# Kernel tuning notes

Measured on AMD Instinct MI355X. Metric: run time of the kernel, lower is better.

## Reference

```python
import jax, jax.numpy as jnp
import numpy as np

B, S, H, NH, NE = 4, 1024, 256, 4, 4
D = H // NH  # head_unit = 64
EPS = 1e-8


def layernorm(x, g, b):
    m = jnp.mean(x, axis=-1, keepdims=True)
    v = jnp.mean((x - m) ** 2, axis=-1, keepdims=True)
    return (x - m) / jnp.sqrt(v + EPS) * g + b


def setup_inputs() -> dict:
    key = jax.random.key(0)
    ks = jax.random.split(key, 18)
    sc = 0.05
    return {
        "x": jax.random.normal(ks[0], (B, S, H), jnp.float32),
        # MoEMultiHead params
        "hl_w": jax.random.normal(ks[1], (NH, D, H), jnp.float32) * sc,   # head_layer weights (out,in)
        "hl_b": jax.random.normal(ks[2], (NH, D), jnp.float32) * sc,
        "wq": jax.random.normal(ks[3], (NH, NE, D, D), jnp.float32) * sc,  # w_q[i*NH+j] -> wq[i,j]
        "wk": jax.random.normal(ks[4], (NH, D, D), jnp.float32) * sc,
        "wv": jax.random.normal(ks[5], (NH, D, D), jnp.float32) * sc,
        "gate_w": jax.random.normal(ks[6], (NH, NE, NE * D), jnp.float32) * sc,
        "gate_b": jax.random.normal(ks[7], (NH, NE), jnp.float32) * sc,
        "ln_g": jnp.ones((D,), jnp.float32),
        "ln_b": jnp.zeros((D,), jnp.float32),
        # FFN params (built inside forward in torch; materialized here)
        "fc1_w": jax.random.normal(ks[8], (D, D), jnp.float32) * sc,
        "fc1_b": jax.random.normal(ks[9], (D,), jnp.float32) * sc,
        "fc2_w": jax.random.normal(ks[10], (D, D), jnp.float32) * sc,
        "fc2_b": jax.random.normal(ks[11], (D,), jnp.float32) * sc,
        "fnorm_g": jnp.ones((D,), jnp.float32),
        "fnorm_b": jnp.zeros((D,), jnp.float32),
        "fgate_w": jax.random.normal(ks[12], (NH, H), jnp.float32) * sc,
    }


def reference(x, hl_w, hl_b, wq, wk, wv, gate_w, gate_b, ln_g, ln_b,
              fc1_w, fc1_b, fc2_w, fc2_b, fnorm_g, fnorm_b, fgate_w):
    b, s, h = x.shape
    nh, d, _ = wk.shape
    ne = wq.shape[1]
    # per-head projection of full hidden -> head_unit  (B, NH, S, D)
    sx = jnp.einsum('bsh,ndh->bnsd', x, hl_w) + hl_b[None, :, None, :]
    pad = sx == 0  # padding mask, same for all experts
    # per-(head, expert) q; per-head k, v
    q = jnp.einsum('bnsd,neod->bneso', sx, wq)       # (B,NH,NE,S,D)
    k = jnp.einsum('bnsd,nod->bnso', sx, wk)         # (B,NH,S,D)
    v = jnp.einsum('bnsd,nod->bnso', sx, wv)
    causal = jnp.where(jnp.tril(jnp.ones((s, s), bool)), 0.0, -jnp.inf).astype(x.dtype)
    # NOTE: original MULTIPLIES by sqrt(head_unit) (bug-faithful)
    scores = jnp.einsum('bnesd,bntd->bnest', q, k) * (d ** 0.5) + causal
    att = jax.nn.softmax(scores, axis=-1)
    qkv = jnp.einsum('bnest,bntd->bnesd', att, v)
    qkv = jnp.where(pad[:, :, None], 0.0, qkv)
    # concat experts along feature dim: (B,NH,S,NE*D)
    out = jnp.transpose(qkv, (0, 1, 3, 2, 4)).reshape(b, nh, s, ne * d)
    gs = jax.nn.softmax(jnp.einsum('bnsf,nef->bnse', out, gate_w) + gate_b[None, :, None, :], axis=-1)
    mixed = jnp.einsum('bnsed,bnse->bnsd', out.reshape(b, nh, s, ne, d), gs)
    # bug-faithful residual: split_x[i] indexes the BATCH dim with head index i
    resid = sx[jnp.arange(nh), jnp.arange(nh)]  # (NH, S, D), broadcast over batch
    hn = layernorm(mixed + resid, ln_g, ln_b)   # (B,NH,S,D); dropout inactive (p=0)
    f_n = jnp.transpose(hn, (0, 2, 1, 3)).reshape(b, s, h)
    # ---- FFN (fresh module in torch; deterministic params here) ----
    fx = f_n.reshape(b, s, nh, d)  # torch.split along feature dim
    pm = fx == 0
    hx = jnp.where(pm, 0.0, fx @ fc1_w.T + fc1_b)
    hx = jax.nn.relu(hx)
    hx = jnp.where(pm, 0.0, hx @ fc2_w.T + fc2_b)
    hx = layernorm(hx + fx, fnorm_g, fnorm_b)
    fout = hx.reshape(b, s, h)
    fg = jax.nn.softmax(fout @ fgate_w.T, axis=-1)  # (B,S,NH)
    return (fout.reshape(b, s, nh, d) * fg[..., None]).reshape(b, s, h)
```

## Files before the change

### kernel.cpp

```cpp
#include <hip/hip_runtime.h>
#include <math.h>

typedef unsigned short u16;
typedef __attribute__((ext_vector_type(8))) unsigned short us8;
typedef __attribute__((ext_vector_type(4))) unsigned short us4;
typedef __attribute__((ext_vector_type(8))) short bf16x8;
typedef __attribute__((ext_vector_type(4))) float f32x4;

constexpr int B_ = 4, S_ = 1024, H_ = 256, NH_ = 4, NE_ = 4, D_ = 64;
constexpr float EPS_ = 1e-8f;

__device__ __forceinline__ u16 f2bf(float f){
  unsigned u = __float_as_uint(f);
  unsigned rnd = 0x7fffu + ((u>>16)&1u);
  return (u16)((u + rnd)>>16);
}
__device__ __forceinline__ us8 pack8(float4 a, float4 b){
  us8 r;
  r[0]=f2bf(a.x); r[1]=f2bf(a.y); r[2]=f2bf(a.z); r[3]=f2bf(a.w);
  r[4]=f2bf(b.x); r[5]=f2bf(b.y); r[6]=f2bf(b.z); r[7]=f2bf(b.w);
  return r;
}
#define MFMA16(a,b,c) __builtin_amdgcn_mfma_f32_16x16x32_bf16((bf16x8)(a),(bf16x8)(b),(c),0,0,0)

__global__ __launch_bounds__(256) void k_sx(const float* __restrict__ x, const float* __restrict__ hlw,
                                            const float* __restrict__ hlb,
                                            float* __restrict__ sx, u16* __restrict__ sxb){
  int mt = blockIdx.x >> 3, nt = blockIdx.x & 7;
  int tid = threadIdx.x, w = tid>>6, l = tid&63, lr = l>>4, lc = l&15;
  __shared__ u16 Xs[64*64];
  __shared__ u16 Ws[32*64];
  const int swl = (lc&7)<<3;
  f32x4 acc[2] = {{0,0,0,0},{0,0,0,0}};
  for(int ks=0; ks<4; ++ks){
    __syncthreads();
    #pragma unroll
    for(int it=0; it<2; ++it){
      int c0 = w*8 + it*32;
      const float* xp = x + ((size_t)(mt*64+l))*H_ + ks*64 + c0;
      float4 a = *(const float4*)xp, b = *(const float4*)(xp+4);
      *(us8*)&Xs[l*64 + (c0 ^ ((l&7)<<3))] = pack8(a,b);
    }
    { int row = tid&31, c0 = (tid>>5)*8;
      const float* wp = hlw + ((size_t)(nt*32+row))*H_ + ks*64 + c0;
      float4 a = *(const float4*)wp, b = *(const float4*)(wp+4);
      *(us8*)&Ws[row*64 + (c0 ^ ((row&7)<<3))] = pack8(a,b);
    }
    __syncthreads();
    bf16x8 a0 = *(const bf16x8*)&Xs[(w*16+lc)*64 + ((lr*8   ) ^ swl)];
    bf16x8 a1 = *(const bf16x8*)&Xs[(w*16+lc)*64 + ((lr*8+32) ^ swl)];
    #pragma unroll
    for(int j=0;j<2;j++){
      const u16* wr = &Ws[(j*16+lc)*64];
      bf16x8 b0 = *(const bf16x8*)(wr + ((lr*8   ) ^ swl));
      bf16x8 b1 = *(const bf16x8*)(wr + ((lr*8+32) ^ swl));
      acc[j] = MFMA16(a0,b0,acc[j]);
      acc[j] = MFMA16(a1,b1,acc[j]);
    }
  }
  #pragma unroll
  for(int j=0;j<2;j++){
    int col = nt*32 + j*16 + lc;
    int n = col>>6, d = col&63;
    float bias = hlb[col];
    #pragma unroll
    for(int r=0;r<4;r++){
      int m = mt*64 + w*16 + lr*4 + r;
      int b = m>>10, s = m&1023;
      float v = acc[j][r] + bias;
      size_t idx = ((size_t)(b*NH_+n)*S_ + s)*D_ + d;
      sx[idx] = v; sxb[idx] = f2bf(v);
    }
  }
}

__global__ __launch_bounds__(256) void k_qkv(const u16* __restrict__ sxb, const float* __restrict__ wq,
            const float* __restrict__ wk, const float* __restrict__ wv,
            u16* __restrict__ qb, u16* __restrict__ kbf, u16* __restrict__ vbf){
  int bid = blockIdx.x;
  int half = bid&1, mt = (bid>>1)&63, n = bid>>7;
  int tid = threadIdx.x, w = tid>>6, l = tid&63, lr = l>>4, lc = l&15;
  __shared__ u16 As[64*64];
  __shared__ u16 Ws[192*64];
  const int swl = (lc&7)<<3;
  int b = (mt*64)>>10, s0 = (mt*64)&1023;
  #pragma unroll
  for(int it=0; it<2; ++it){
    int c0 = w*8 + it*32;
    us8 v = *(const us8*)(sxb + ((size_t)(b*NH_+n)*S_ + s0 + l)*D_ + c0);
    *(us8*)&As[l*64 + (c0 ^ ((l&7)<<3))] = v;
  }
  #pragma unroll
  for(int ch=0; ch<3; ++ch){
    int o = half*192 + ch*64 + l;
    const float* src;
    if(o < 256)      src = wq + ((size_t)((n*NE_ + (o>>6))*D_ + (o&63)))*D_;
    else if(o < 320) src = wk + ((size_t)(n*D_ + (o-256)))*D_;
    else             src = wv + ((size_t)(n*D_ + (o-320)))*D_;
    #pragma unroll
    for(int it=0; it<2; ++it){
      int c0 = w*8 + it*32;
      float4 a = *(const float4*)(src+c0), bb = *(const float4*)(src+c0+4);
      *(us8*)&Ws[(ch*64+l)*64 + (c0 ^ ((l&7)<<3))] = pack8(a,bb);
    }
  }
  __syncthreads();
  bf16x8 a0 = *(const bf16x8*)&As[(w*16+lc)*64 + ((lr*8   ) ^ swl)];
  bf16x8 a1 = *(const bf16x8*)&As[(w*16+lc)*64 + ((lr*8+32) ^ swl)];
  f32x4 acc[12];
  #pragma unroll
  for(int j=0;j<12;j++) acc[j] = (f32x4){0,0,0,0};
  #pragma unroll
  for(int j=0;j<12;j++){
    const u16* wr = &Ws[(j*16+lc)*64];
    bf16x8 b0 = *(const bf16x8*)(wr + ((lr*8   ) ^ swl));
    bf16x8 b1 = *(const bf16x8*)(wr + ((lr*8+32) ^ swl));
    acc[j] = MFMA16(a0,b0,acc[j]);
    acc[j] = MFMA16(a1,b1,acc[j]);
  }
  #pragma unroll
  for(int j=0;j<12;j++){
    int o = half*192 + j*16 + lc;
    #pragma unroll
    for(int r=0;r<4;r++){
      int s = s0 + w*16 + lr*4 + r;
      float v = acc[j][r];
      if(o < 256){
        int e = o>>6, d = o&63;
        qb[((size_t)((b*NH_+n)*NE_+e)*S_ + s)*D_ + d] = f2bf(v*8.f);
      } else if(o < 320){
        kbf[((size_t)(b*NH_+n)*S_ + s)*D_ + (o-256)] = f2bf(v);
      } else {
        vbf[((size_t)(b*NH_+n)*S_ + s)*D_ + (o-320)] = f2bf(v);
      }
    }
  }
}

__global__ __launch_bounds__(256) void k_attn(const u16* __restrict__ qb, const u16* __restrict__ kb,
        const u16* __restrict__ vb, const float* __restrict__ sx, float* __restrict__ attout){
  int bid = blockIdx.x;
  int head = bid>>3, p = bid&7;
  int bq = head>>2, e = head&3;
  int tid = threadIdx.x, w = tid>>6, l = tid&63, lr = l>>4, lc = l&15;
  __shared__ u16 Ks[2][64*64];
  __shared__ u16 VT[2][64*64];
  __shared__ u16 Pb[4][16*64];
  const u16* kh = kb + (size_t)bq*S_*D_;
  const u16* vh = vb + (size_t)bq*S_*D_;
  const int swl = (lc&7)<<3;
  const int swst = (l&7)<<3;

  #pragma unroll
  for(int ph=0; ph<2; ++ph){
    int qt = ph ? (15-p) : p;
    const u16* qrow = qb + ((size_t)head*S_ + qt*64 + w*16 + lc)*D_;
    bf16x8 qf0 = *(const bf16x8*)(qrow + lr*8);
    bf16x8 qf1 = *(const bf16x8*)(qrow + lr*8 + 32);
    f32x4 Oa[4]; float m_i[4], l_i[4];
    #pragma unroll
    for(int j=0;j<4;j++) Oa[j] = (f32x4){0,0,0,0};
    #pragma unroll
    for(int r=0;r<4;r++){ m_i[r] = -INFINITY; l_i[r] = 0.f; }

    us8 rg[4];
    __syncthreads();
    { const u16* kr = kh + (size_t)l*D_;
      const u16* vr = vh + (size_t)l*D_;
      int c0 = w*8;
      rg[0] = *(const us8*)(kr + c0);      rg[1] = *(const us8*)(kr + c0 + 32);
      rg[2] = *(const us8*)(vr + c0);      rg[3] = *(const us8*)(vr + c0 + 32);
      *(us8*)&Ks[0][l*64 + ( c0      ^ swst)] = rg[0];
      *(us8*)&Ks[0][l*64 + ((c0+32)  ^ swst)] = rg[1];
      #pragma unroll
      for(int i=0;i<8;i++){ int d=c0+i;    VT[0][d*64 + (l ^ ((d&7)<<3))] = rg[2][i]; }
      #pragma unroll
      for(int i=0;i<8;i++){ int d=c0+32+i; VT[0][d*64 + (l ^ ((d&7)<<3))] = rg[3][i]; }
    }
    for(int kt=0; kt<=qt; ++kt){
      int cur = kt&1;
      __syncthreads();
      bool more = kt < qt;
      if(more){
        const u16* kr = kh + ((size_t)(kt+1)*64 + l)*D_;
        const u16* vr = vh + ((size_t)(kt+1)*64 + l)*D_;
        int c0 = w*8;
        rg[0] = *(const us8*)(kr + c0);    rg[1] = *(const us8*)(kr + c0 + 32);
        rg[2] = *(const us8*)(vr + c0);    rg[3] = *(const us8*)(vr + c0 + 32);
      }
      f32x4 Sa[4];
      #pragma unroll
      for(int j=0;j<4;j++){
        const u16* kr = &Ks[cur][(j*16+lc)*64];
        bf16x8 b0 = *(const bf16x8*)(kr + ((lr*8   ) ^ swl));
        bf16x8 b1 = *(const bf16x8*)(kr + ((lr*8+32) ^ swl));
        f32x4 z = (f32x4){0,0,0,0};
        z = MFMA16(qf0,b0,z);
        z = MFMA16(qf1,b1,z);
        Sa[j] = z;
      }
      #pragma unroll
      for(int r=0;r<4;r++){
        int qr = w*16 + lr*4 + r;
        float sv[4];
        #pragma unroll
        for(int j=0;j<4;j++){
          sv[j] = Sa[j][r];
          if(kt==qt && (j*16+lc) > qr) sv[j] = -INFINITY;
        }
        float mx = fmaxf(fmaxf(sv[0],sv[1]),fmaxf(sv[2],sv[3]));
        #pragma unroll
        for(int off=1; off<16; off<<=1) mx = fmaxf(mx, __shfl_xor(mx,off));
        float mn = fmaxf(m_i[r], mx);
        float sc = __expf(m_i[r]-mn);
        float rs = 0.f;
        #pragma unroll
        for(int j=0;j<4;j++){ sv[j] = __expf(sv[j]-mn); rs += sv[j]; }
        #pragma unroll
        for(int off=1; off<16; off<<=1) rs += __shfl_xor(rs,off);
        l_i[r] = l_i[r]*sc + rs;
        m_i[r] = mn;
        #pragma unroll
        for(int j=0;j<4;j++) Oa[j][r] *= sc;
        int prow = lr*4+r, psw = (prow&7)<<3;
        #pragma unroll
        for(int j=0;j<4;j++) Pb[w][prow*64 + ((j*16+lc) ^ psw)] = f2bf(sv[j]);
      }
      asm volatile("s_waitcnt lgkmcnt(0)" ::: "memory");
      bf16x8 pA0 = *(const bf16x8*)&Pb[w][lc*64 + ((lr*8   ) ^ swl)];
      bf16x8 pA1 = *(const bf16x8*)&Pb[w][lc*64 + ((lr*8+32) ^ swl)];
      #pragma unroll
      for(int jd=0;jd<4;jd++){
        const u16* vr = &VT[cur][(jd*16+lc)*64];
        bf16x8 v0 = *(const bf16x8*)(vr + ((lr*8   ) ^ swl));
        bf16x8 v1 = *(const bf16x8*)(vr + ((lr*8+32) ^ swl));
        Oa[jd] = MFMA16(pA0,v0,Oa[jd]);
        Oa[jd] = MFMA16(pA1,v1,Oa[jd]);
      }
      if(more){
        int nb = cur^1, c0 = w*8;
        *(us8*)&Ks[nb][l*64 + ( c0     ^ swst)] = rg[0];
        *(us8*)&Ks[nb][l*64 + ((c0+32) ^ swst)] = rg[1];
        #pragma unroll
        for(int i=0;i<8;i++){ int d=c0+i;    VT[nb][d*64 + (l ^ ((d&7)<<3))] = rg[2][i]; }
        #pragma unroll
        for(int i=0;i<8;i++){ int d=c0+32+i; VT[nb][d*64 + (l ^ ((d&7)<<3))] = rg[3][i]; }
      }
    }
    #pragma unroll
    for(int r=0;r<4;r++){
      int qg = qt*64 + w*16 + lr*4 + r;
      float inv = 1.f/l_i[r];
      #pragma unroll
      for(int jd=0;jd<4;jd++){
        int d = jd*16 + lc;
        float o = Oa[jd][r]*inv;
        if(sx[((size_t)bq*S_ + qg)*D_ + d] == 0.f) o = 0.f;
        attout[((size_t)bq*S_ + qg)*(NE_*D_) + e*D_ + d] = o;
      }
    }
  }
}

__global__ __launch_bounds__(256) void k_tail(const float* __restrict__ attout, const float* __restrict__ gw,
      const float* __restrict__ gb, const float* __restrict__ sx,
      const float* __restrict__ lng, const float* __restrict__ lnb,
      const float* __restrict__ w1g, const float* __restrict__ b1g,
      const float* __restrict__ w2g, const float* __restrict__ b2g,
      const float* __restrict__ fng, const float* __restrict__ fnb,
      const float* __restrict__ fgw, float* __restrict__ out){
  int bid = blockIdx.x;
  int gs0 = bid*16, b = gs0>>10, s0 = gs0&1023;
  int tid = threadIdx.x;
  int row = tid>>4, l16 = tid&15;
  int w = tid>>6, l = tid&63, lr = l>>4, lc = l&15;
  __shared__ float Fx[64][64];
  __shared__ u16 FnB[64*64];
  __shared__ u16 W1[64*64], W2[64*64], H1[64*64];
  __shared__ float Red[4][16][4];

  #pragma unroll
  for(int g2=0; g2<2; ++g2){
    int g = tid*2+g2; int r2 = g>>3, c0 = (g&7)*8;
    float4 a = *(const float4*)(w1g + r2*64 + c0), bb = *(const float4*)(w1g + r2*64 + c0 + 4);
    *(us8*)&W1[r2*64 + (c0 ^ ((r2&7)<<3))] = pack8(a,bb);
    a = *(const float4*)(w2g + r2*64 + c0); bb = *(const float4*)(w2g + r2*64 + c0 + 4);
    *(us8*)&W2[r2*64 + (c0 ^ ((r2&7)<<3))] = pack8(a,bb);
  }
  const int d0 = l16*4;
  for(int n=0;n<NH_;++n){
    f32x4 o[4];
    const float* ar = attout + ((size_t)(b*NH_+n)*S_ + s0 + row)*(NE_*D_);
    #pragma unroll
    for(int e=0;e<4;e++) o[e] = *(const f32x4*)(ar + e*64 + d0);
    float lg4[4];
    #pragma unroll
    for(int eg=0; eg<4; ++eg){
      const float* gr = gw + (size_t)(n*NE_+eg)*(NE_*D_);
      float p = 0.f;
      #pragma unroll
      for(int e=0;e<4;e++){
        f32x4 g4 = *(const f32x4*)(gr + e*64 + d0);
        p += o[e][0]*g4[0] + o[e][1]*g4[1] + o[e][2]*g4[2] + o[e][3]*g4[3];
      }
      #pragma unroll
      for(int off=1; off<16; off<<=1) p += __shfl_xor(p, off);
      lg4[eg] = p + gb[n*NE_+eg];
    }
    float mx = fmaxf(fmaxf(lg4[0],lg4[1]),fmaxf(lg4[2],lg4[3]));
    float se = 0.f;
    #pragma unroll
    for(int eg=0;eg<4;eg++){ lg4[eg]=__expf(lg4[eg]-mx); se+=lg4[eg]; }
    float inv = 1.f/se;
    f32x4 res = *(const f32x4*)(sx + ((size_t)(n*NH_+n)*S_ + s0 + row)*D_ + d0);
    float tv[4];
    #pragma unroll
    for(int k=0;k<4;k++){
      float mixk = o[0][k]*lg4[0] + o[1][k]*lg4[1] + o[2][k]*lg4[2] + o[3][k]*lg4[3];
      tv[k] = mixk*inv + res[k];
    }
    float sum = tv[0]+tv[1]+tv[2]+tv[3];
    #pragma unroll
    for(int off=1; off<16; off<<=1) sum += __shfl_xor(sum, off);
    float mean = sum*(1.f/64.f);
    float vs = 0.f;
    #pragma unroll
    for(int k=0;k<4;k++){ float d = tv[k]-mean; vs += d*d; }
    #pragma unroll
    for(int off=1; off<16; off<<=1) vs += __shfl_xor(vs, off);
    float rstd = rsqrtf(vs*(1.f/64.f)+EPS_);
    f32x4 lgv = *(const f32x4*)(lng + d0);
    f32x4 lbv = *(const f32x4*)(lnb + d0);
    int hr = n*16+row;
    us4 pk;
    f32x4 yv;
    #pragma unroll
    for(int k=0;k<4;k++){
      float y = (tv[k]-mean)*rstd*lgv[k] + lbv[k];
      yv[k] = y; pk[k] = f2bf(y);
    }
    *(f32x4*)&Fx[hr][d0] = yv;
    *(us4*)&FnB[hr*64 + (d0 ^ ((hr&7)<<3))] = pk;
  }
  __syncthreads();
  const int swl = (lc&7)<<3;
  bf16x8 a0 = *(const bf16x8*)&FnB[(w*16+lc)*64 + ((lr*8   ) ^ swl)];
  bf16x8 a1 = *(const bf16x8*)&FnB[(w*16+lc)*64 + ((lr*8+32) ^ swl)];
  f32x4 acc1[4];
  #pragma unroll
  for(int jn=0;jn<4;jn++) acc1[jn] = (f32x4){0,0,0,0};
  #pragma unroll
  for(int jn=0;jn<4;jn++){
    const u16* wr = &W1[(jn*16+lc)*64];
    bf16x8 b0 = *(const bf16x8*)(wr + ((lr*8   ) ^ swl));
    bf16x8 b1 = *(const bf16x8*)(wr + ((lr*8+32) ^ swl));
    acc1[jn] = MFMA16(a0,b0,acc1[jn]);
    acc1[jn] = MFMA16(a1,b1,acc1[jn]);
  }
  #pragma unroll
  for(int jn=0;jn<4;jn++){
    int dout = jn*16+lc;
    float bias = b1g[dout];
    #pragma unroll
    for(int rr=0;rr<4;rr++){
      int hr = w*16 + lr*4 + rr;
      float v = acc1[jn][rr] + bias;
      v = (Fx[hr][dout]==0.f) ? 0.f : v;
      v = fmaxf(v, 0.f);
      H1[hr*64 + (dout ^ ((hr&7)<<3))] = f2bf(v);
    }
  }
  __syncthreads();
  a0 = *(const bf16x8*)&H1[(w*16+lc)*64 + ((lr*8   ) ^ swl)];
  a1 = *(const bf16x8*)&H1[(w*16+lc)*64 + ((lr*8+32) ^ swl)];
  f32x4 acc2[4];
  #pragma unroll
  for(int jn=0;jn<4;jn++) acc2[jn] = (f32x4){0,0,0,0};
  #pragma unroll
  for(int jn=0;jn<4;jn++){
    const u16* wr = &W2[(jn*16+lc)*64];
    bf16x8 b0 = *(const bf16x8*)(wr + ((lr*8   ) ^ swl));
    bf16x8 b1 = *(const bf16x8*)(wr + ((lr*8+32) ^ swl));
    acc2[jn] = MFMA16(a0,b0,acc2[jn]);
    acc2[jn] = MFMA16(a1,b1,acc2[jn]);
  }
  float tv2[4][4];
  #pragma unroll
  for(int jn=0;jn<4;jn++){
    int dout = jn*16+lc;
    float bias = b2g[dout];
    #pragma unroll
    for(int rr=0;rr<4;rr++){
      int hr = w*16 + lr*4 + rr;
      float fx = Fx[hr][dout];
      float v = acc2[jn][rr] + bias;
      v = (fx==0.f) ? 0.f : v;
      tv2[jn][rr] = v + fx;
    }
  }
  float sum_r[4], vs_r[4];
  #pragma unroll
  for(int rr=0;rr<4;rr++) sum_r[rr] = tv2[0][rr]+tv2[1][rr]+tv2[2][rr]+tv2[3][rr];
  #pragma unroll
  for(int off=1; off<16; off<<=1)
    #pragma unroll
    for(int rr=0;rr<4;rr++) sum_r[rr] += __shfl_xor(sum_r[rr], off);
  float mean_r[4];
  #pragma unroll
  for(int rr=0;rr<4;rr++) mean_r[rr] = sum_r[rr]*(1.f/64.f);
  #pragma unroll
  for(int rr=0;rr<4;rr++){
    float a = tv2[0][rr]-mean_r[rr], b2v = tv2[1][rr]-mean_r[rr];
    float c = tv2[2][rr]-mean_r[rr], d = tv2[3][rr]-mean_r[rr];
    vs_r[rr] = a*a + b2v*b2v + c*c + d*d;
  }
  #pragma unroll
  for(int off=1; off<16; off<<=1)
    #pragma unroll
    for(int rr=0;rr<4;rr++) vs_r[rr] += __shfl_xor(vs_r[rr], off);
  float y2[4][4];
  #pragma unroll
  for(int jn=0;jn<4;jn++){
    int dout = jn*16+lc;
    float g = fng[dout], bb = fnb[dout];
    #pragma unroll
    for(int rr=0;rr<4;rr++){
      float rstd = rsqrtf(vs_r[rr]*(1.f/64.f)+EPS_);
      y2[jn][rr] = (tv2[jn][rr]-mean_r[rr])*rstd*g + bb;
    }
  }
  float fg4[4][4];
  #pragma unroll
  for(int j=0;j<4;j++)
    #pragma unroll
    for(int jn=0;jn<4;jn++)
      fg4[j][jn] = fgw[(size_t)j*H_ + w*64 + jn*16 + lc];
  float pj[4][4];
  #pragma unroll
  for(int j=0;j<4;j++)
    #pragma unroll
    for(int rr=0;rr<4;rr++)
      pj[j][rr] = y2[0][rr]*fg4[j][0] + y2[1][rr]*fg4[j][1] + y2[2][rr]*fg4[j][2] + y2[3][rr]*fg4[j][3];
  #pragma unroll
  for(int off=1; off<16; off<<=1)
    #pragma unroll
    for(int j=0;j<4;j++)
      #pragma unroll
      for(int rr=0;rr<4;rr++) pj[j][rr] += __shfl_xor(pj[j][rr], off);
  if(lc==0){
    #pragma unroll
    for(int rr=0;rr<4;rr++)
      #pragma unroll
      for(int j=0;j<4;j++) Red[w][lr*4+rr][j] = pj[j][rr];
  }
  __syncthreads();
  #pragma unroll
  for(int rr=0;rr<4;rr++){
    int srow = lr*4+rr;
    float lgf[4];
    #pragma unroll
    for(int j=0;j<4;j++) lgf[j] = Red[0][srow][j]+Red[1][srow][j]+Red[2][srow][j]+Red[3][srow][j];
    float mx2 = fmaxf(fmaxf(lgf[0],lgf[1]),fmaxf(lgf[2],lgf[3]));
    float se2 = 0.f;
    #pragma unroll
    for(int j=0;j<4;j++){ lgf[j]=__expf(lgf[j]-mx2); se2+=lgf[j]; }
    float gsn = lgf[w]/se2;
    float* op = out + ((size_t)(gs0 + srow))*H_ + w*64;
    #pragma unroll
    for(int jn=0;jn<4;jn++) op[jn*16+lc] = y2[jn][rr]*gsn;
  }
}

extern "C" void kernel_launch(void* const* d_in, const int* in_sizes, int n_in,
                              void* d_out, int out_size, void* d_ws, size_t ws_size,
                              hipStream_t stream){
  const float* x      = (const float*)d_in[0];
  const float* hl_w   = (const float*)d_in[1];
  const float* hl_b   = (const float*)d_in[2];
  const float* wq     = (const float*)d_in[3];
  const float* wk     = (const float*)d_in[4];
  const float* wv     = (const float*)d_in[5];
  const float* gate_w = (const float*)d_in[6];
  const float* gate_b = (const float*)d_in[7];
  const float* ln_g   = (const float*)d_in[8];
  const float* ln_b   = (const float*)d_in[9];
  const float* fc1_w  = (const float*)d_in[10];
  const float* fc1_b  = (const float*)d_in[11];
  const float* fc2_w  = (const float*)d_in[12];
  const float* fc2_b  = (const float*)d_in[13];
  const float* fnorm_g= (const float*)d_in[14];
  const float* fnorm_b= (const float*)d_in[15];
  const float* fgate_w= (const float*)d_in[16];

  const size_t NSD = (size_t)B_*NH_*S_*D_;
  float* ws     = (float*)d_ws;
  float* sx     = ws;
  float* attout = sx + NSD;
  float* f_n    = attout + NSD*NE_;
  u16*   sxb    = (u16*)(f_n + NSD);
  u16*   qb     = sxb + NSD;
  u16*   kbf    = qb + NSD*NE_;
  u16*   vbf    = kbf + NSD;

  k_sx  <<<512,  256, 0, stream>>>(x, hl_w, hl_b, sx, sxb);
  k_qkv <<<512,  256, 0, stream>>>(sxb, wq, wk, wv, qb, kbf, vbf);
  k_attn<<<512,  256, 0, stream>>>(qb, kbf, vbf, sx, attout);
  k_tail<<<256,  256, 0, stream>>>(attout, gate_w, gate_b, sx, ln_g, ln_b,
                                   fc1_w, fc1_b, fc2_w, fc2_b,
                                   fnorm_g, fnorm_b, fgate_w, (float*)d_out);
}
```

Measured before the change: 73.99 us.

## Restructure causal attention: one q-tile per block, transposed S, exp2 softmax

The attention kernel now launches one block per (head, query tile) instead of pairing two tiles per block, and interleaves tile assignment so heavy and light causal tiles are spread across the grid. It computes S transposed (K as the A operand) so each lane owns one query row, which cuts the row reductions to two cross-lane shuffles and lets P be stored with packed 4-wide writes. It folds log2(e) into the Q scale so the softmax can use exp2f, and it vectorizes the masked output store. Launch bounds request higher occupancy; the risk is more blocks each reloading Q and register pressure from the occupancy hint.

```diff
diff --git a/kernel.cpp b/kernel.cpp
--- a/kernel.cpp
+++ b/kernel.cpp
@@ -68,7 +68,7 @@
       int m = mt*64 + w*16 + lr*4 + r;
       int b = m>>10, s = m&1023;
       float v = acc[j][r] + bias;
-      size_t idx = ((size_t)(b*NH_+n)*S_ + s)*D_ + d;
+      size_t idx = ((size_t)(b*NH_+n)*S_+s)*D_ + d;
       sx[idx] = v; sxb[idx] = f2bf(v);
     }
   }
@@ -127,7 +127,7 @@
       float v = acc[j][r];
       if(o < 256){
         int e = o>>6, d = o&63;
-        qb[((size_t)((b*NH_+n)*NE_+e)*S_ + s)*D_ + d] = f2bf(v*8.f);
+        qb[((size_t)((b*NH_+n)*NE_+e)*S_ + s)*D_ + d] = f2bf(v*11.5415603f);
       } else if(o < 320){
         kbf[((size_t)(b*NH_+n)*S_ + s)*D_ + (o-256)] = f2bf(v);
       } else {
@@ -137,10 +137,12 @@
   }
 }
 
-__global__ __launch_bounds__(256) void k_attn(const u16* __restrict__ qb, const u16* __restrict__ kb,
+__global__ __launch_bounds__(256,4) void k_attn(const u16* __restrict__ qb, const u16* __restrict__ kb,
         const u16* __restrict__ vb, const float* __restrict__ sx, float* __restrict__ attout){
   int bid = blockIdx.x;
-  int head = bid>>3, p = bid&7;
+  int head = bid & 63, idx = bid >> 6;
+  int g = idx>>2, pos = idx&3;
+  int qt = (g&1) ? (15 - (g>>1) - 2*pos) : ((g>>1) + 2*pos);
   int bq = head>>2, e = head&3;
   int tid = threadIdx.x, w = tid>>6, l = tid&63, lr = l>>4, lc = l&15;
   __shared__ u16 Ks[2][64*64];
@@ -151,114 +153,127 @@
   const int swl = (lc&7)<<3;
   const int swst = (l&7)<<3;
 
-  #pragma unroll
-  for(int ph=0; ph<2; ++ph){
-    int qt = ph ? (15-p) : p;
-    const u16* qrow = qb + ((size_t)head*S_ + qt*64 + w*16 + lc)*D_;
-    bf16x8 qf0 = *(const bf16x8*)(qrow + lr*8);
-    bf16x8 qf1 = *(const bf16x8*)(qrow + lr*8 + 32);
-    f32x4 Oa[4]; float m_i[4], l_i[4];
-    #pragma unroll
-    for(int j=0;j<4;j++) Oa[j] = (f32x4){0,0,0,0};
-    #pragma unroll
-    for(int r=0;r<4;r++){ m_i[r] = -INFINITY; l_i[r] = 0.f; }
-
-    us8 rg[4];
+  const u16* qrow = qb + ((size_t)head*S_ + qt*64 + w*16 + lc)*D_;
+  bf16x8 qf0 = *(const bf16x8*)(qrow + lr*8);
+  bf16x8 qf1 = *(const bf16x8*)(qrow + lr*8 + 32);
+  f32x4 Oa[4];
+  #pragma unroll
+  for(int j=0;j<4;j++) Oa[j] = (f32x4){0,0,0,0};
+  float m_i = -INFINITY, l_i = 0.f;
+
+  us8 rg[4];
+  {
+    const u16* kr = kh + (size_t)l*D_;
+    const u16* vr = vh + (size_t)l*D_;
+    int c0 = w*8;
+    rg[0] = *(const us8*)(kr + c0);      rg[1] = *(const us8*)(kr + c0 + 32);
+    rg[2] = *(const us8*)(vr + c0);      rg[3] = *(const us8*)(vr + c0 + 32);
+    *(us8*)&Ks[0][l*64 + ( c0      ^ swst)] = rg[0];
+    *(us8*)&Ks[0][l*64 + ((c0+32)  ^ swst)] = rg[1];
+    #pragma unroll
+    for(int i=0;i<8;i++){ int d=c0+i;    VT[0][d*64 + (l ^ ((d&7)<<3))] = rg[2][i]; }
+    #pragma unroll
+    for(int i=0;i<8;i++){ int d=c0+32+i; VT[0][d*64 + (l ^ ((d&7)<<3))] = rg[3][i]; }
+  }
+  for(int kt=0; kt<=qt; ++kt){
+    int cur = kt&1;
     __syncthreads();
-    { const u16* kr = kh + (size_t)l*D_;
-      const u16* vr = vh + (size_t)l*D_;
+    bool more = kt < qt;
+    if(more){
+      const u16* kr = kh + ((size_t)(kt+1)*64 + l)*D_;
+      const u16* vr = vh + ((size_t)(kt+1)*64 + l)*D_;
       int c0 = w*8;
-      rg[0] = *(const us8*)(kr + c0);      rg[1] = *(const us8*)(kr + c0 + 32);
-      rg[2] = *(const us8*)(vr + c0);      rg[3] = *(const us8*)(vr + c0 + 32);
-      *(us8*)&Ks[0][l*64 + ( c0      ^ swst)] = rg[0];
-      *(us8*)&Ks[0][l*64 + ((c0+32)  ^ swst)] = rg[1];
-      #pragma unroll
-      for(int i=0;i<8;i++){ int d=c0+i;    VT[0][d*64 + (l ^ ((d&7)<<3))] = rg[2][i]; }
-      #pragma unroll
-      for(int i=0;i<8;i++){ int d=c0+32+i; VT[0][d*64 + (l ^ ((d&7)<<3))] = rg[3][i]; }
-    }
-    for(int kt=0; kt<=qt; ++kt){
-      int cur = kt&1;
-      __syncthreads();
-      bool more = kt < qt;
-      if(more){
-        const u16* kr = kh + ((size_t)(kt+1)*64 + l)*D_;
-        const u16* vr = vh + ((size_t)(kt+1)*64 + l)*D_;
-        int c0 = w*8;
-        rg[0] = *(const us8*)(kr + c0);    rg[1] = *(const us8*)(kr + c0 + 32);
-        rg[2] = *(const us8*)(vr + c0);    rg[3] = *(const us8*)(vr + c0 + 32);
-      }
-      f32x4 Sa[4];
-      #pragma unroll
-      for(int j=0;j<4;j++){
-        const u16* kr = &Ks[cur][(j*16+lc)*64];
-        bf16x8 b0 = *(const bf16x8*)(kr + ((lr*8   ) ^ swl));
-        bf16x8 b1 = *(const bf16x8*)(kr + ((lr*8+32) ^ swl));
-        f32x4 z = (f32x4){0,0,0,0};
-        z = MFMA16(qf0,b0,z);
-        z = MFMA16(qf1,b1,z);
-        Sa[j] = z;
-      }
-      #pragma unroll
-      for(int r=0;r<4;r++){
-        int qr = w*16 + lr*4 + r;
-        float sv[4];
+      rg[0] = *(const us8*)(kr + c0);    rg[1] = *(const us8*)(kr + c0 + 32);
+      rg[2] = *(const us8*)(vr + c0);    rg[3] = *(const us8*)(vr + c0 + 32);
+    }
+    f32x4 Sa[4];
+    #pragma unroll
+    for(int j=0;j<4;j++){
+      const u16* kr = &Ks[cur][(j*16+lc)*64];
+      bf16x8 a0 = *(const bf16x8*)(kr + ((lr*8   ) ^ swl));
+      bf16x8 a1 = *(const bf16x8*)(kr + ((lr*8+32) ^ swl));
+      f32x4 z = (f32x4){0,0,0,0};
+      z = MFMA16(a0,qf0,z);
+      z = MFMA16(a1,qf1,z);
+      Sa[j] = z;
+    }
+    if(kt==qt){
+      int q = w*16 + lc;
+      #pragma unroll
+      for(int j=0;j<4;j++)
         #pragma unroll
-        for(int j=0;j<4;j++){
-          sv[j] = Sa[j][r];
-          if(kt==qt && (j*16+lc) > qr) sv[j] = -INFINITY;
-        }
-        float mx = fmaxf(fmaxf(sv[0],sv[1]),fmaxf(sv[2],sv[3]));
-        #pragma unroll
-        for(int off=1; off<16; off<<=1) mx = fmaxf(mx, __shfl_xor(mx,off));
-        float mn = fmaxf(m_i[r], mx);
-        float sc = __expf(m_i[r]-mn);
-        float rs = 0.f;
-        #pragma unroll
-        for(int j=0;j<4;j++){ sv[j] = __expf(sv[j]-mn); rs += sv[j]; }
-        #pragma unroll
-        for(int off=1; off<16; off<<=1) rs += __shfl_xor(rs,off);
-        l_i[r] = l_i[r]*sc + rs;
-        m_i[r] = mn;
-        #pragma unroll
-        for(int j=0;j<4;j++) Oa[j][r] *= sc;
-        int prow = lr*4+r, psw = (prow&7)<<3;
-        #pragma unroll
-        for(int j=0;j<4;j++) Pb[w][prow*64 + ((j*16+lc) ^ psw)] = f2bf(sv[j]);
-      }
-      asm volatile("s_waitcnt lgkmcnt(0)" ::: "memory");
-      bf16x8 pA0 = *(const bf16x8*)&Pb[w][lc*64 + ((lr*8   ) ^ swl)];
-      bf16x8 pA1 = *(const bf16x8*)&Pb[w][lc*64 + ((lr*8+32) ^ swl)];
-      #pragma unroll
-      for(int jd=0;jd<4;jd++){
-        const u16* vr = &VT[cur][(jd*16+lc)*64];
-        bf16x8 v0 = *(const bf16x8*)(vr + ((lr*8   ) ^ swl));
-        bf16x8 v1 = *(const bf16x8*)(vr + ((lr*8+32) ^ swl));
-        Oa[jd] = MFMA16(pA0,v0,Oa[jd]);
-        Oa[jd] = MFMA16(pA1,v1,Oa[jd]);
-      }
-      if(more){
-        int nb = cur^1, c0 = w*8;
-        *(us8*)&Ks[nb][l*64 + ( c0     ^ swst)] = rg[0];
-        *(us8*)&Ks[nb][l*64 + ((c0+32) ^ swst)] = rg[1];
-        #pragma unroll
-        for(int i=0;i<8;i++){ int d=c0+i;    VT[nb][d*64 + (l ^ ((d&7)<<3))] = rg[2][i]; }
-        #pragma unroll
-        for(int i=0;i<8;i++){ int d=c0+32+i; VT[nb][d*64 + (l ^ ((d&7)<<3))] = rg[3][i]; }
-      }
-    }
+        for(int r=0;r<4;r++)
+          if(j*16 + lr*4 + r > q) Sa[j][r] = -INFINITY;
+    }
+    float mx0 = fmaxf(fmaxf(Sa[0][0],Sa[0][1]),fmaxf(Sa[0][2],Sa[0][3]));
+    float mx1 = fmaxf(fmaxf(Sa[1][0],Sa[1][1]),fmaxf(Sa[1][2],Sa[1][3]));
+    float mx2 = fmaxf(fmaxf(Sa[2][0],Sa[2][1]),fmaxf(Sa[2][2],Sa[2][3]));
+    float mx3 = fmaxf(fmaxf(Sa[3][0],Sa[3][1]),fmaxf(Sa[3][2],Sa[3][3]));
+    float mx = fmaxf(fmaxf(mx0,mx1),fmaxf(mx2,mx3));
+    mx = fmaxf(mx, __shfl_xor(mx,16));
+    mx = fmaxf(mx, __shfl_xor(mx,32));
+    float mn = fmaxf(m_i, mx);
+    float scale = exp2f(m_i - mn);
+    #pragma unroll
+    for(int j=0;j<4;j++)
+      #pragma unroll
+      for(int r=0;r<4;r++) Sa[j][r] = exp2f(Sa[j][r] - mn);
+    float rs0 = (Sa[0][0]+Sa[0][1]) + (Sa[0][2]+Sa[0][3]);
+    float rs1 = (Sa[1][0]+Sa[1][1]) + (Sa[1][2]+Sa[1][3]);
+    float rs2 = (Sa[2][0]+Sa[2][1]) + (Sa[2][2]+Sa[2][3]);
+    float rs3 = (Sa[3][0]+Sa[3][1]) + (Sa[3][2]+Sa[3][3]);
+    float rs = (rs0+rs1) + (rs2+rs3);
+    rs += __shfl_xor(rs,16);
+    rs += __shfl_xor(rs,32);
+    l_i = l_i*scale + rs;
+    m_i = mn;
+    #pragma unroll
+    for(int jd=0;jd<4;jd++)
+      #pragma unroll
+      for(int r=0;r<4;r++) Oa[jd][r] *= scale;
+    #pragma unroll
+    for(int j=0;j<4;j++){
+      us4 pk;
+      #pragma unroll
+      for(int r=0;r<4;r++) pk[r] = f2bf(Sa[j][r]);
+      *(us4*)&Pb[w][lc*64 + ((j*16+lr*4) ^ swl)] = pk;
+    }
+    asm volatile("s_waitcnt lgkmcnt(0)" ::: "memory");
+    bf16x8 pB0 = *(const bf16x8*)&Pb[w][lc*64 + ((lr*8   ) ^ swl)];
+    bf16x8 pB1 = *(const bf16x8*)&Pb[w][lc*64 + ((lr*8+32) ^ swl)];
+    #pragma unroll
+    for(int jd=0;jd<4;jd++){
+      const u16* vr = &VT[cur][(jd*16+lc)*64];
+      bf16x8 v0 = *(const bf16x8*)(vr + ((lr*8   ) ^ swl));
+      bf16x8 v1 = *(const bf16x8*)(vr + ((lr*8+32) ^ swl));
+      Oa[jd] = MFMA16(v0,pB0,Oa[jd]);
+      Oa[jd] = MFMA16(v1,pB1,Oa[jd]);
+    }
+    if(more){
+      int nb = cur^1, c0 = w*8;
+      *(us8*)&Ks[nb][l*64 + ( c0     ^ swst)] = rg[0];
+      *(us8*)&Ks[nb][l*64 + ((c0+32) ^ swst)] = rg[1];
+      #pragma unroll
+      for(int i=0;i<8;i++){ int d=c0+i;    VT[nb][d*64 + (l ^ ((d&7)<<3))] = rg[2][i]; }
+      #pragma unroll
+      for(int i=0;i<8;i++){ int d=c0+32+i; VT[nb][d*64 + (l ^ ((d&7)<<3))] = rg[3][i]; }
+    }
+  }
+  int qg = qt*64 + w*16 + lc;
+  float inv = 1.f/l_i;
+  const float* sxp = sx + ((size_t)bq*S_ + qg)*D_;
+  float* op = attout + ((size_t)bq*S_ + qg)*(NE_*D_) + e*D_;
+  #pragma unroll
+  for(int jd=0;jd<4;jd++){
+    int d0 = jd*16 + lr*4;
+    f32x4 sxv = *(const f32x4*)(sxp + d0);
+    f32x4 ov;
     #pragma unroll
     for(int r=0;r<4;r++){
-      int qg = qt*64 + w*16 + lr*4 + r;
-      float inv = 1.f/l_i[r];
-      #pragma unroll
-      for(int jd=0;jd<4;jd++){
-        int d = jd*16 + lc;
-        float o = Oa[jd][r]*inv;
-        if(sx[((size_t)bq*S_ + qg)*D_ + d] == 0.f) o = 0.f;
-        attout[((size_t)bq*S_ + qg)*(NE_*D_) + e*D_ + d] = o;
-      }
-    }
+      float o = Oa[jd][r]*inv;
+      ov[r] = (sxv[r]==0.f) ? 0.f : o;
+    }
+    *(f32x4*)(op + d0) = ov;
   }
 }
 
@@ -504,7 +519,7 @@
 
   k_sx  <<<512,  256, 0, stream>>>(x, hl_w, hl_b, sx, sxb);
   k_qkv <<<512,  256, 0, stream>>>(sxb, wq, wk, wv, qb, kbf, vbf);
-  k_attn<<<512,  256, 0, stream>>>(qb, kbf, vbf, sx, attout);
+  k_attn<<<1024, 256, 0, stream>>>(qb, kbf, vbf, sx, attout);
   k_tail<<<256,  256, 0, stream>>>(attout, gate_w, gate_b, sx, ln_g, ln_b,
                                    fc1_w, fc1_b, fc2_w, fc2_b,
                                    fnorm_g, fnorm_b, fgate_w, (float*)d_out);
```

New measurement: 67.06 us. 1.1x faster.
